# Performance work log

Hardware: AMD Instinct MI355X
Metric: run time of the kernel (lower is better)

Reference implementation:

```python
import jax, jax.numpy as jnp
import numpy as np

DEPTH, DIM, HEADS, MLP_HID, POS_DIM, PROJ_DIM, NCLS, INP = 5, 128, 8, 256, 128, 128, 1000, 35
EPS = 1e-5

def _ln(x, g, b):
    m = x.mean(-1, keepdims=True)
    v = ((x - m) ** 2).mean(-1, keepdims=True)
    return (x - m) / jnp.sqrt(v + EPS) * g + b

def _gelu(x):
    return jax.nn.gelu(x, approximate=False)  # torch nn.GELU default (erf)

def setup_inputs() -> dict:
    key = jax.random.key(0)
    ks = iter(jax.random.split(key, 80))
    nxt = lambda: next(ks)
    B, N = 8, 1024
    w = lambda *s: (jax.random.normal(nxt(), s, jnp.float32) / np.sqrt(s[-2]).astype(np.float32))
    z = lambda *s: jnp.zeros(s, jnp.float32)
    o = lambda *s: jnp.ones(s, jnp.float32)
    node_feat = jax.random.normal(nxt(), (B, N, 3), jnp.float32)
    a = (jax.random.uniform(nxt(), (B, N, N)) < 0.01).astype(jnp.float32)
    adj = jnp.maximum(a, a.transpose(0, 2, 1))  # symmetric 0/1 adjacency
    lapl = jax.random.normal(nxt(), (B, N, 32), jnp.float32) * 0.1
    d = dict(
        node_feat=node_feat, adj=adj, lapl=lapl,
        cls_token=jax.random.normal(nxt(), (1, 1, DIM), jnp.float32),
        pe_w1=w(INP, 2 * INP), pe_b1=z(2 * INP),
        pe_w2=w(2 * INP, 2 * INP), pe_b2=z(2 * INP),
        pe_w3=w(2 * INP, 2 * INP), pe_b3=z(2 * INP),
        pe_lng=o(2 * INP), pe_lnb=z(2 * INP),
        pe_w4=w(2 * INP, POS_DIM), pe_b4=z(POS_DIM),
        blk_ln1_g=o(DEPTH, DIM), blk_ln1_b=z(DEPTH, DIM),
        blk_qkv_w=w(DEPTH, DIM, 3 * HEADS * DIM),
        blk_proj_w=w(DEPTH, HEADS * DIM, DIM), blk_proj_b=z(DEPTH, DIM),
        blk_gamma_w=jax.random.uniform(nxt(), (DEPTH, DIM, 2), jnp.float32) * 0.01,
        blk_gamma_b=z(DEPTH, 2),
        blk_ln2_g=o(DEPTH, DIM), blk_ln2_b=z(DEPTH, DIM),
        blk_mlp_w1=w(DEPTH, DIM, MLP_HID), blk_mlp_b1=z(DEPTH, MLP_HID),
        blk_mlp_w2=w(DEPTH, MLP_HID, DIM), blk_mlp_b2=z(DEPTH, DIM),
        head_lng=o(DIM), head_lnb=z(DIM), head_w=w(DIM, DIM), head_b=z(DIM),
        proj_w1=w(DIM, PROJ_DIM), proj_b1=z(PROJ_DIM),
        proj_w2=w(PROJ_DIM, PROJ_DIM), proj_b2=z(PROJ_DIM),
        proj_w3=w(PROJ_DIM, PROJ_DIM), proj_b3=z(PROJ_DIM),
        proj_lng=o(PROJ_DIM), proj_lnb=z(PROJ_DIM),
        proj_w4=w(PROJ_DIM, NCLS), proj_b4=z(NCLS),
    )
    return d

def reference(node_feat, adj, lapl, cls_token, pe_w1, pe_b1, pe_w2, pe_b2, pe_w3, pe_b3,
              pe_lng, pe_lnb, pe_w4, pe_b4, blk_ln1_g, blk_ln1_b, blk_qkv_w, blk_proj_w,
              blk_proj_b, blk_gamma_w, blk_gamma_b, blk_ln2_g, blk_ln2_b, blk_mlp_w1,
              blk_mlp_b1, blk_mlp_w2, blk_mlp_b2, head_lng, head_lnb, head_w, head_b,
              proj_w1, proj_b1, proj_w2, proj_b2, proj_w3, proj_b3, proj_lng, proj_lnb,
              proj_w4, proj_b4):
    B, N, _ = node_feat.shape
    M = N + 1
    # positional-encoding MLP on concatenated [node_feat | lapl] (inp_dim = 35)
    x = jnp.concatenate([node_feat, lapl], axis=2)
    x = _gelu(x @ pe_w1 + pe_b1)
    x = _gelu(x @ pe_w2 + pe_b2)
    x = _gelu(x @ pe_w3 + pe_b3)
    x = _ln(x, pe_lng, pe_lnb) @ pe_w4 + pe_b4  # [B,N,DIM]
    x = jnp.concatenate([jnp.broadcast_to(cls_token, (B, 1, DIM)), x], axis=1)  # [B,M,DIM]
    # adjacency with cls row/col, adj_cls[:,0,0] = 1
    adj_cls = jnp.zeros((B, M, M), x.dtype).at[:, 0, 0].set(1.0).at[:, 1:, 1:].set(adj)
    scale = DIM ** (-0.5)
    for i in range(DEPTH):
        h = _ln(x, blk_ln1_g[i], blk_ln1_b[i])
        qkv = (h @ blk_qkv_w[i]).reshape(B, M, 3, HEADS, DIM).transpose(2, 0, 3, 1, 4)
        q, k, v = qkv[0], qkv[1], qkv[2]  # each [B,H,M,D]
        attn = jnp.einsum('bhnd,bhmd->bhnm', q, k) * scale
        gamma = jnp.exp(h @ blk_gamma_w[i] + blk_gamma_b[i])  # [B,M,2], use_exp=True
        attn = gamma[:, None, :, 0:1] * attn + gamma[:, None, :, 1:2] * adj_cls[:, None]
        attn = jax.nn.softmax(attn, axis=-1)
        o = jnp.einsum('bhnm,bhmd->bhnd', attn, v).transpose(0, 2, 1, 3).reshape(B, M, HEADS * DIM)
        x = o @ blk_proj_w[i] + blk_proj_b[i] + h  # residual from normed input (as in source)
        h2 = _ln(x, blk_ln2_g[i], blk_ln2_b[i])
        x = _gelu(h2 @ blk_mlp_w1[i] + blk_mlp_b1[i]) @ blk_mlp_w2[i] + blk_mlp_b2[i] + h2
    c = x[:, 0]
    c = _ln(c, head_lng, head_lnb) @ head_w + head_b  # mlp_head
    p = _gelu(c @ proj_w1 + proj_b1)
    p = _gelu(p @ proj_w2 + proj_b2)
    p = _gelu(p @ proj_w3 + proj_b3)
    p = _ln(p, proj_lng, proj_lnb) @ proj_w4 + proj_b4
    return (c, p)
```

## Files before the change

### kernel.cpp

```cpp
#include <hip/hip_runtime.h>
#include <hip/hip_bf16.h>
#include <math.h>

#define NB 8
#define NSEQ 1024
#define M_ 1025
#define ROWS (NB * M_)
#define DIMC 128
#define NHEADS 8
#define QKV3 3072
#define PEROWS (NB * NSEQ)
#define ACS 1088

typedef __attribute__((ext_vector_type(8))) short bf16x8;
typedef __attribute__((ext_vector_type(4))) float f32x4;

__device__ __forceinline__ float gelu_f(float x) {
  return 0.5f * x * (1.f + erff(x * 0.70710678118654752440f));
}

__device__ __forceinline__ unsigned short f2bf(float f) {
  __hip_bfloat16 h = __float2bfloat16(f);
  return *reinterpret_cast<unsigned short*>(&h);
}

__device__ __forceinline__ float bf2f(unsigned short u) {
  union { unsigned int i; float f; } c;
  c.i = ((unsigned int)u) << 16;
  return c.f;
}

__device__ __forceinline__ void g2lds16(const void* g, void* l) {
  __builtin_amdgcn_global_load_lds(
      (__attribute__((address_space(1))) void*)(g),
      (__attribute__((address_space(3))) void*)(l), 16, 0, 0);
}

template<int K, int KP, int C, int SS, int DOGELU>
__device__ __forceinline__ void pe_stage(
    int tid, const float* __restrict__ W, const float* __restrict__ B,
    const float* src, float* dst, float (*wb)[128])
{
  for (int i = tid; i < K * C; i += 128) wb[i / C][i % C] = W[i];
  if (tid < C) {
#pragma unroll
    for (int k = K; k < KP; ++k) wb[k][tid] = 0.f;
  }
  __syncthreads();
  if (tid < C) {
    float acc[16];
#pragma unroll
    for (int r = 0; r < 16; ++r) acc[r] = B[tid];
#pragma unroll 1
    for (int k4 = 0; k4 < KP; k4 += 4) {
      const float w0 = wb[k4 + 0][tid];
      const float w1 = wb[k4 + 1][tid];
      const float w2 = wb[k4 + 2][tid];
      const float w3 = wb[k4 + 3][tid];
#pragma unroll
      for (int r = 0; r < 16; ++r) {
        const float4 av = *(const float4*)&src[r * SS + k4];
        acc[r] = fmaf(av.x, w0, acc[r]);
        acc[r] = fmaf(av.y, w1, acc[r]);
        acc[r] = fmaf(av.z, w2, acc[r]);
        acc[r] = fmaf(av.w, w3, acc[r]);
      }
    }
#pragma unroll
    for (int r = 0; r < 16; ++r) dst[r * 72 + tid] = DOGELU ? gelu_f(acc[r]) : acc[r];
  }
  __syncthreads();
}

__global__ __launch_bounds__(128) void pe_fused_k(
    const float* __restrict__ nf, const float* __restrict__ lp,
    const float* __restrict__ w1, const float* __restrict__ b1,
    const float* __restrict__ w2, const float* __restrict__ b2,
    const float* __restrict__ w3, const float* __restrict__ b3,
    const float* __restrict__ lng, const float* __restrict__ lnb,
    const float* __restrict__ w4, const float* __restrict__ b4,
    float* __restrict__ x)
{
  __shared__ float sIn[16][36];
  __shared__ float sX[16][72];
  __shared__ float sY[16][72];
  __shared__ float wb[72][128];
  const int tid = threadIdx.x;
  const int r0 = blockIdx.x * 16;

  for (int i = tid; i < 16 * 35; i += 128) {
    const int r = i / 35, c = i - r * 35;
    const int gr = r0 + r;
    sIn[r][c] = (c < 3) ? nf[(size_t)gr * 3 + c] : lp[(size_t)gr * 32 + (c - 3)];
  }
  if (tid < 16) {
    sIn[tid][35] = 0.f;
    sX[tid][70] = 0.f; sX[tid][71] = 0.f;
    sY[tid][70] = 0.f; sY[tid][71] = 0.f;
  }
  __syncthreads();

  pe_stage<35, 36, 70, 36, 1>(tid, w1, b1, &sIn[0][0], &sX[0][0], wb);
  pe_stage<70, 72, 70, 72, 1>(tid, w2, b2, &sX[0][0], &sY[0][0], wb);
  pe_stage<70, 72, 70, 72, 1>(tid, w3, b3, &sY[0][0], &sX[0][0], wb);

  if (tid < 16) {
    float m = 0.f;
    for (int d = 0; d < 70; ++d) m += sX[tid][d];
    m *= (1.f / 70.f);
    float v = 0.f;
    for (int d = 0; d < 70; ++d) { const float t = sX[tid][d] - m; v += t * t; }
    const float inv = rsqrtf(v * (1.f / 70.f) + 1e-5f);
    for (int d = 0; d < 70; ++d) sX[tid][d] = (sX[tid][d] - m) * inv * lng[d] + lnb[d];
  }
  __syncthreads();

  {
    for (int i = tid; i < 70 * 128; i += 128) wb[i >> 7][i & 127] = w4[i];
#pragma unroll
    for (int k = 70; k < 72; ++k) wb[k][tid] = 0.f;
    __syncthreads();
    float acc[16];
#pragma unroll
    for (int r = 0; r < 16; ++r) acc[r] = b4[tid];
#pragma unroll 1
    for (int k4 = 0; k4 < 72; k4 += 4) {
      const float w0 = wb[k4 + 0][tid];
      const float w1v = wb[k4 + 1][tid];
      const float w2v = wb[k4 + 2][tid];
      const float w3v = wb[k4 + 3][tid];
#pragma unroll
      for (int r = 0; r < 16; ++r) {
        const float4 av = *(const float4*)&sX[r][k4];
        acc[r] = fmaf(av.x, w0, acc[r]);
        acc[r] = fmaf(av.y, w1v, acc[r]);
        acc[r] = fmaf(av.z, w2v, acc[r]);
        acc[r] = fmaf(av.w, w3v, acc[r]);
      }
    }
#pragma unroll
    for (int r = 0; r < 16; ++r) {
      const int gr = r0 + r;
      x[(size_t)(gr + gr / 1024 + 1) * DIMC + tid] = acc[r];
    }
  }
}

template<int ACT, int OBF, int RES>
__global__ __launch_bounds__(256) void mgemm_k(
    const unsigned short* __restrict__ Xb, const unsigned short* __restrict__ Wt,
    const float* __restrict__ bias, const float* __restrict__ res,
    void* __restrict__ outp, int rows, int K, int N)
{
  __shared__ unsigned short sX[64][72];
  __shared__ unsigned short sW[64][72];
  const int tid = threadIdx.x;
  const int w = tid >> 6, lane = tid & 63;
  const int col = lane & 15, quad = lane >> 4;
  const int r0 = blockIdx.x * 64, n0 = blockIdx.y * 64;
  const int lr = tid >> 2, lc = tid & 3;
  const int xrow = min(r0 + lr, rows - 1);
  const unsigned short* xsrc = Xb + (size_t)xrow * K + lc * 8;
  const unsigned short* wsrc = Wt + (size_t)(n0 + lr) * K + lc * 8;

  f32x4 acc[4];
#pragma unroll
  for (int t = 0; t < 4; ++t) acc[t] = (f32x4){0.f, 0.f, 0.f, 0.f};

  for (int k0 = 0; k0 < K; k0 += 64) {
    __syncthreads();
    *(uint4*)&sX[lr][lc * 8]      = *(const uint4*)(xsrc + k0);
    *(uint4*)&sX[lr][lc * 8 + 32] = *(const uint4*)(xsrc + k0 + 32);
    *(uint4*)&sW[lr][lc * 8]      = *(const uint4*)(wsrc + k0);
    *(uint4*)&sW[lr][lc * 8 + 32] = *(const uint4*)(wsrc + k0 + 32);
    __syncthreads();
    const bf16x8 aX0 = *(const bf16x8*)&sX[w * 16 + col][quad * 8];
    const bf16x8 aX1 = *(const bf16x8*)&sX[w * 16 + col][32 + quad * 8];
#pragma unroll
    for (int t = 0; t < 4; ++t) {
      const bf16x8 bW0 = *(const bf16x8*)&sW[t * 16 + col][quad * 8];
      const bf16x8 bW1 = *(const bf16x8*)&sW[t * 16 + col][32 + quad * 8];
      acc[t] = __builtin_amdgcn_mfma_f32_16x16x32_bf16(aX0, bW0, acc[t], 0, 0, 0);
      acc[t] = __builtin_amdgcn_mfma_f32_16x16x32_bf16(aX1, bW1, acc[t], 0, 0, 0);
    }
  }
  const int gr_base = r0 + w * 16 + quad * 4;
#pragma unroll
  for (int t = 0; t < 4; ++t) {
    const int n = n0 + t * 16 + col;
    const float bv = bias ? bias[n] : 0.f;
#pragma unroll
    for (int r = 0; r < 4; ++r) {
      const int gr = gr_base + r;
      if (gr < rows) {
        float v = acc[t][r] + bv;
        if (ACT) v = gelu_f(v);
        if (RES) v += res[(size_t)gr * N + n];
        if (OBF) ((unsigned short*)outp)[(size_t)gr * N + n] = f2bf(v);
        else     ((float*)outp)[(size_t)gr * N + n] = v;
      }
    }
  }
}

template<int OBF, int VT>
__global__ __launch_bounds__(256) void mgemm128_k(
    const unsigned short* __restrict__ Xb, const unsigned short* __restrict__ Wt,
    const float* __restrict__ bias, void* __restrict__ outp,
    unsigned short* __restrict__ vtp, int rows, int K, int N)
{
  __shared__ unsigned short sX[128][72];
  __shared__ unsigned short sW[128][72];
  const int tid = threadIdx.x;
  const int w = tid >> 6, lane = tid & 63;
  const int col = lane & 15, quad = lane >> 4;
  const int wr = w >> 1, wc = w & 1;
  const int r0 = blockIdx.x * 128, n0 = blockIdx.y * 128;

  f32x4 acc[4][4];
#pragma unroll
  for (int i = 0; i < 4; ++i)
#pragma unroll
    for (int j = 0; j < 4; ++j) acc[i][j] = (f32x4){0.f, 0.f, 0.f, 0.f};

  for (int k0 = 0; k0 < K; k0 += 64) {
    __syncthreads();
#pragma unroll
    for (int l = 0; l < 4; ++l) {
      const int idx = l * 256 + tid;
      const int row = idx >> 3, c = idx & 7;
      const int xrow = min(r0 + row, rows - 1);
      *(uint4*)&sX[row][c * 8] = *(const uint4*)(Xb + (size_t)xrow * K + k0 + c * 8);
      *(uint4*)&sW[row][c * 8] = *(const uint4*)(Wt + (size_t)(n0 + row) * K + k0 + c * 8);
    }
    __syncthreads();
    bf16x8 aX[4][2];
#pragma unroll
    for (int i = 0; i < 4; ++i) {
      aX[i][0] = *(const bf16x8*)&sX[wr * 64 + i * 16 + col][quad * 8];
      aX[i][1] = *(const bf16x8*)&sX[wr * 64 + i * 16 + col][32 + quad * 8];
    }
#pragma unroll
    for (int j = 0; j < 4; ++j) {
      const bf16x8 b0 = *(const bf16x8*)&sW[wc * 64 + j * 16 + col][quad * 8];
      const bf16x8 b1 = *(const bf16x8*)&sW[wc * 64 + j * 16 + col][32 + quad * 8];
#pragma unroll
      for (int i = 0; i < 4; ++i) {
        acc[i][j] = __builtin_amdgcn_mfma_f32_16x16x32_bf16(aX[i][0], b0, acc[i][j], 0, 0, 0);
        acc[i][j] = __builtin_amdgcn_mfma_f32_16x16x32_bf16(aX[i][1], b1, acc[i][j], 0, 0, 0);
      }
    }
  }
  const bool dovt = VT && (n0 >= 2048);
#pragma unroll
  for (int i = 0; i < 4; ++i) {
    const int gr_base = r0 + wr * 64 + i * 16 + quad * 4;
    int bb[4], mm[4];
    if (dovt) {
#pragma unroll
      for (int r = 0; r < 4; ++r) {
        const int gr = gr_base + r;
        bb[r] = gr / 1025;
        mm[r] = gr - bb[r] * 1025;
      }
    }
#pragma unroll
    for (int j = 0; j < 4; ++j) {
      const int n = n0 + wc * 64 + j * 16 + col;
      const float bv = bias ? bias[n] : 0.f;
      const int hh = (n - 2048) >> 7;
      const int d  = (n - 2048) & 127;
#pragma unroll
      for (int r = 0; r < 4; ++r) {
        const int gr = gr_base + r;
        if (gr < rows) {
          const float v = acc[i][j][r] + bv;
          const unsigned short bf = f2bf(v);
          if (OBF) ((unsigned short*)outp)[(size_t)gr * N + n] = bf;
          else     ((float*)outp)[(size_t)gr * N + n] = v;
          if (dovt) vtp[(((size_t)(bb[r] * NHEADS + hh) * DIMC + d) * ACS) + mm[r]] = bf;
        }
      }
    }
  }
}

__global__ __launch_bounds__(256) void ln_rows_k(
    const float* __restrict__ in, float* __restrict__ out,
    unsigned short* __restrict__ outb,
    const float* __restrict__ g, const float* __restrict__ b,
    const float* __restrict__ gw, const float* __restrict__ gb,
    float* __restrict__ gamout, int rows, int D)
{
  const int wv = (blockIdx.x * blockDim.x + threadIdx.x) >> 6;
  const int lane = threadIdx.x & 63;
  if (wv >= rows) return;
  const float* r = in + (size_t)wv * D;
  float s = 0.f;
  for (int d = lane; d < D; d += 64) s += r[d];
  for (int off = 32; off; off >>= 1) s += __shfl_down(s, off);
  const float mean = __shfl(s, 0) / (float)D;
  float v = 0.f;
  for (int d = lane; d < D; d += 64) { float t = r[d] - mean; v += t * t; }
  for (int off = 32; off; off >>= 1) v += __shfl_down(v, off);
  const float inv = rsqrtf(__shfl(v, 0) / (float)D + 1e-5f);
  float* orow = out + (size_t)wv * D;
  float a0 = 0.f, a1 = 0.f;
  for (int d = lane; d < D; d += 64) {
    const float o = (r[d] - mean) * inv * g[d] + b[d];
    orow[d] = o;
    if (outb) outb[(size_t)wv * D + d] = f2bf(o);
    if (gw) { a0 = fmaf(o, gw[2 * d], a0); a1 = fmaf(o, gw[2 * d + 1], a1); }
  }
  if (gw) {
    for (int off = 32; off; off >>= 1) { a0 += __shfl_down(a0, off); a1 += __shfl_down(a1, off); }
    if (lane == 0) {
      gamout[(size_t)wv * 2 + 0] = expf(a0 + gb[0]);
      gamout[(size_t)wv * 2 + 1] = expf(a1 + gb[1]);
    }
  }
}

__global__ __launch_bounds__(256) void adjp_k(const float* __restrict__ adj,
                                              unsigned long long* __restrict__ adjp)
{
  const int n = blockIdx.x;
  const int b = blockIdx.y;
  const int wv = threadIdx.x >> 6, lane = threadIdx.x & 63;
  for (int w = wv; w < 17; w += 4) {
    const int m = w * 64 + lane;
    float av = 0.f;
    if (n == 0) av = (m == 0) ? 1.f : 0.f;
    else if (m >= 1 && m <= NSEQ) av = adj[((size_t)b * NSEQ + (n - 1)) * NSEQ + (m - 1)];
    const unsigned long long mask = __ballot(av != 0.f);
    if (lane == 0) adjp[((size_t)b * M_ + n) * 17 + w] = mask;
  }
}

__global__ void wtrans_k(const float* __restrict__ W, unsigned short* __restrict__ Wt,
                         int K, int N)
{
  __shared__ float t[32][33];
  const int k0 = blockIdx.x * 32, n0 = blockIdx.y * 32;
  const float* Wd = W + (size_t)blockIdx.z * K * N;
  unsigned short* Wtd = Wt + (size_t)blockIdx.z * K * N;
  for (int i = threadIdx.y; i < 32; i += 8)
    t[i][threadIdx.x] = Wd[(size_t)(k0 + i) * N + n0 + threadIdx.x];
  __syncthreads();
  for (int i = threadIdx.y; i < 32; i += 8)
    Wtd[(size_t)(n0 + i) * K + k0 + threadIdx.x] = f2bf(t[threadIdx.x][i]);
}

__global__ __launch_bounds__(512) void attn_mfma_k(
    const unsigned short* __restrict__ qkv, const float* __restrict__ gamma,
    const unsigned long long* __restrict__ adjp, const unsigned short* __restrict__ vt,
    unsigned short* __restrict__ o)
{
  __shared__ unsigned short sK[2][64][128];
  __shared__ unsigned short sVt[2][128][64];
  __shared__ unsigned short sP[256][64];

  const int hh = blockIdx.x, qt = blockIdx.y, b = blockIdx.z;
  const int tid = threadIdx.x;
  const int w = tid >> 6;
  const int lane = tid & 63;
  const int col = lane & 15;
  const int quad = lane >> 4;
  const int qbase = qt * 256 + w * 32;
  const float scale = 0.088388347648318447f;

  bf16x8 aQ[2][4];
#pragma unroll
  for (int rg = 0; rg < 2; ++rg) {
    const int qrow = qbase + rg * 16 + col;
    const unsigned short* qp = qkv + ((size_t)(b * M_ + qrow)) * QKV3 + hh * DIMC + quad * 8;
#pragma unroll
    for (int c = 0; c < 4; ++c) aQ[rg][c] = *(const bf16x8*)(qp + c * 32);
  }
  float g0[2][4], g1[2][4];
  int adjo[2][4];
#pragma unroll
  for (int rg = 0; rg < 2; ++rg)
#pragma unroll
    for (int r = 0; r < 4; ++r) {
      const int nc = qbase + rg * 16 + quad * 4 + r;
      g0[rg][r] = gamma[(size_t)(b * M_ + nc) * 2 + 0] * scale;
      g1[rg][r] = gamma[(size_t)(b * M_ + nc) * 2 + 1];
      adjo[rg][r] = (b * M_ + nc) * 17;
    }

  float l_i[2][4] = {{0.f, 0.f, 0.f, 0.f}, {0.f, 0.f, 0.f, 0.f}};
  f32x4 Oacc[2][8];
#pragma unroll
  for (int rg = 0; rg < 2; ++rg)
#pragma unroll
    for (int t = 0; t < 8; ++t) Oacc[rg][t] = (f32x4){0.f, 0.f, 0.f, 0.f};

  const size_t vtbase = ((size_t)(b * NHEADS + hh)) * DIMC * ACS;

  auto stageK = [&](int buf, int kt_) {
#pragma unroll
    for (int l = 0; l < 2; ++l) {
      const int m = l * 32 + w * 4 + (lane >> 4);
      const int gm = min(kt_ * 64 + m, 1024);
      const unsigned short* src = qkv + ((size_t)(b * M_ + gm)) * QKV3 + 1024
                                  + hh * DIMC + (((lane & 15) ^ (m & 7)) * 8);
      g2lds16(src, &sK[buf][l * 32 + w * 4][0]);
    }
  };
  auto stageV = [&](int buf, int kt_) {
#pragma unroll
    for (int l = 0; l < 2; ++l) {
      const int d = l * 64 + w * 8 + (lane >> 3);
      const unsigned short* src = vt + vtbase + (size_t)d * ACS + kt_ * 64
                                  + (((lane & 7) ^ (d & 7)) * 8);
      g2lds16(src, &sVt[buf][l * 64 + w * 8][0]);
    }
  };

  stageK(0, 0);
  stageV(0, 0);

  int cur = 0;
  for (int kt = 0; kt < 17; ++kt) {
    const int m0 = kt * 64;
    asm volatile("s_waitcnt vmcnt(0)" ::: "memory");
    __builtin_amdgcn_s_barrier();
    __builtin_amdgcn_sched_barrier(0);

    const bool more = (kt < 16);
    if (more) {
      stageK(cur ^ 1, kt + 1);
      stageV(cur ^ 1, kt + 1);
    }

    unsigned long long mk[2][4];
#pragma unroll
    for (int rg = 0; rg < 2; ++rg)
#pragma unroll
      for (int r = 0; r < 4; ++r) mk[rg][r] = adjp[adjo[rg][r] + kt];

    f32x4 Sacc[2][4];
#pragma unroll
    for (int rg = 0; rg < 2; ++rg)
#pragma unroll
      for (int t = 0; t < 4; ++t) Sacc[rg][t] = (f32x4){0.f, 0.f, 0.f, 0.f};
    __builtin_amdgcn_s_setprio(1);
#pragma unroll
    for (int t = 0; t < 4; ++t) {
#pragma unroll
      for (int c = 0; c < 4; ++c) {
        const bf16x8 bK = *(const bf16x8*)&sK[cur][t * 16 + col][((c * 4 + quad) ^ (col & 7)) * 8];
        Sacc[0][t] = __builtin_amdgcn_mfma_f32_16x16x32_bf16(aQ[0][c], bK, Sacc[0][t], 0, 0, 0);
        Sacc[1][t] = __builtin_amdgcn_mfma_f32_16x16x32_bf16(aQ[1][c], bK, Sacc[1][t], 0, 0, 0);
      }
    }
    __builtin_amdgcn_s_setprio(0);

#pragma unroll
    for (int t = 0; t < 4; ++t) {
      const int m = m0 + t * 16 + col;
      const bool mv = (m < M_);
      const int chb = t * 2 + (col >> 3);
      const int sh = t * 16 + col;
#pragma unroll
      for (int rg = 0; rg < 2; ++rg)
#pragma unroll
        for (int r = 0; r < 4; ++r) {
          const float bias = ((mk[rg][r] >> sh) & 1ull) ? g1[rg][r] : 0.f;
          const float s = fmaf(g0[rg][r], Sacc[rg][t][r], bias);
          const float pv = mv ? __expf(s) : 0.f;
          l_i[rg][r] += pv;
          const int ql = w * 32 + rg * 16 + quad * 4 + r;
          sP[ql][((chb ^ (ql & 7)) * 8) + (col & 7)] = f2bf(pv);
        }
    }

    __builtin_amdgcn_s_setprio(1);
#pragma unroll
    for (int ch = 0; ch < 2; ++ch) {
      const int pr = w * 32 + col;
      const bf16x8 aP0 = *(const bf16x8*)&sP[pr][((ch * 4 + quad) ^ (col & 7)) * 8];
      const bf16x8 aP1 = *(const bf16x8*)&sP[pr + 16][((ch * 4 + quad) ^ (col & 7)) * 8];
#pragma unroll
      for (int t = 0; t < 8; ++t) {
        const bf16x8 bV = *(const bf16x8*)&sVt[cur][t * 16 + col][((ch * 4 + quad) ^ (col & 7)) * 8];
        Oacc[0][t] = __builtin_amdgcn_mfma_f32_16x16x32_bf16(aP0, bV, Oacc[0][t], 0, 0, 0);
        Oacc[1][t] = __builtin_amdgcn_mfma_f32_16x16x32_bf16(aP1, bV, Oacc[1][t], 0, 0, 0);
      }
    }
    __builtin_amdgcn_s_setprio(0);
    cur ^= 1;
  }

#pragma unroll
  for (int rg = 0; rg < 2; ++rg)
#pragma unroll
    for (int r = 0; r < 4; ++r) {
      float s = l_i[rg][r];
      s += __shfl_xor(s, 1);
      s += __shfl_xor(s, 2);
      s += __shfl_xor(s, 4);
      s += __shfl_xor(s, 8);
      const int n = qbase + rg * 16 + quad * 4 + r;
      const float invl = 1.f / s;
      unsigned short* orow = o + ((size_t)(b * M_ + n)) * (NHEADS * DIMC) + hh * DIMC + col;
#pragma unroll
      for (int t = 0; t < 8; ++t) orow[t * 16] = f2bf(Oacc[rg][t][r] * invl);
    }
}

__global__ __launch_bounds__(256) void cls_attn_k(
    const unsigned short* __restrict__ qkv, const float* __restrict__ gamma,
    const unsigned long long* __restrict__ adjp, const unsigned short* __restrict__ vt,
    unsigned short* __restrict__ o)
{
  __shared__ float qf[DIMC];
  __shared__ float pbuf[1056];
  __shared__ float lred[4];
  __shared__ float oshare[DIMC];
  const int hh = blockIdx.x & 7, b = blockIdx.x >> 3;
  const int tid = threadIdx.x;
  const size_t rowbase = (size_t)b * M_ + 1024;

  if (tid < DIMC) qf[tid] = bf2f(qkv[rowbase * QKV3 + hh * DIMC + tid]);
  __syncthreads();
  const float g0 = gamma[rowbase * 2 + 0] * 0.088388347648318447f;
  const float g1 = gamma[rowbase * 2 + 1];

  float lpart = 0.f;
  for (int m = tid; m < M_; m += 256) {
    const unsigned short* kp = qkv + ((size_t)(b * M_ + m)) * QKV3 + 1024 + hh * DIMC;
    float s = 0.f;
#pragma unroll
    for (int d0 = 0; d0 < DIMC; d0 += 8) {
      const bf16x8 kv = *(const bf16x8*)(kp + d0);
#pragma unroll
      for (int j = 0; j < 8; ++j)
        s = fmaf(bf2f((unsigned short)kv[j]), qf[d0 + j], s);
    }
    const unsigned long long mkv = adjp[rowbase * 17 + (m >> 6)];
    const float bias = ((mkv >> (m & 63)) & 1ull) ? g1 : 0.f;
    const float p = __expf(fmaf(g0, s, bias));
    pbuf[m] = p;
    lpart += p;
  }
  for (int off = 32; off; off >>= 1) lpart += __shfl_down(lpart, off);
  if ((tid & 63) == 0) lred[tid >> 6] = lpart;
  __syncthreads();
  const float linv = 1.f / (lred[0] + lred[1] + lred[2] + lred[3]);

  const int d = tid & 127, half = tid >> 7;
  const unsigned short* vrow = vt + ((size_t)(b * NHEADS + hh)) * DIMC * ACS + (size_t)d * ACS;
  float acc = 0.f;
  const int mstart = half * 512;
  const int mend = half ? 1024 : 512;
  for (int m0 = mstart; m0 < mend; m0 += 8) {
    const bf16x8 vv = *(const bf16x8*)(vrow + m0);
#pragma unroll
    for (int j = 0; j < 8; ++j)
      acc = fmaf(bf2f((unsigned short)vv[j]), pbuf[m0 + j], acc);
  }
  if (half) acc = fmaf(bf2f(vrow[1024]), pbuf[1024], acc);
  if (half == 0) oshare[d] = acc;
  __syncthreads();
  if (half == 1) {
    const float val = (oshare[d] + acc) * linv;
    o[rowbase * (NHEADS * DIMC) + hh * DIMC + d] = f2bf(val);
  }
}

template<int DOLN, int ACT>
__global__ __launch_bounds__(256) void hstage_k(
    const float* __restrict__ in, int in_stride,
    const float* __restrict__ lng, const float* __restrict__ lnb,
    const float* __restrict__ W, const float* __restrict__ bias,
    float* __restrict__ out)
{
  __shared__ float xn[8][128];
  __shared__ float red[128];
  const int tid = threadIdx.x;
  for (int i = tid; i < 1024; i += 256) {
    const int r = i >> 7, d = i & 127;
    xn[r][d] = in[(size_t)r * in_stride + d];
  }
  __syncthreads();
  if (DOLN) {
    const int wv = tid >> 6, lane = tid & 63;
    const int row = wv * 2 + (lane >> 5);
    const int l32 = lane & 31;
    float s = 0.f;
    for (int d = l32; d < 128; d += 32) s += xn[row][d];
    for (int off = 16; off; off >>= 1) s += __shfl_xor(s, off);
    const float mean = s * (1.f / 128.f);
    float v = 0.f;
    for (int d = l32; d < 128; d += 32) { const float t = xn[row][d] - mean; v += t * t; }
    for (int off = 16; off; off >>= 1) v += __shfl_xor(v, off);
    const float inv = rsqrtf(v * (1.f / 128.f) + 1e-5f);
    for (int d = l32; d < 128; d += 32)
      xn[row][d] = (xn[row][d] - mean) * inv * lng[d] + lnb[d];
    __syncthreads();
  }
  const int col = blockIdx.x * 16 + (tid & 15);
  const int row = (tid >> 4) & 7;
  const int ks = tid >> 7;
  float acc = 0.f;
  const int kb = ks * 64;
  for (int k = kb; k < kb + 64; ++k)
    acc = fmaf(xn[row][k], W[k * 128 + col], acc);
  if (ks) red[tid - 128] = acc;
  __syncthreads();
  if (!ks) {
    float v = acc + red[tid] + bias[col];
    if (ACT) v = gelu_f(v);
    out[row * 128 + col] = v;
  }
}

__global__ __launch_bounds__(256) void hfinal_k(
    const float* __restrict__ in,
    const float* __restrict__ plg, const float* __restrict__ plb,
    const float* __restrict__ W, const float* __restrict__ bias,
    float* __restrict__ out_p)
{
  __shared__ float xn[128];
  const int r = blockIdx.x & 7, cc = blockIdx.x >> 3;
  const int tid = threadIdx.x;
  const int lane = tid & 63;
  const float a = in[r * 128 + lane];
  const float b = in[r * 128 + 64 + lane];
  float s = a + b;
  for (int off = 32; off; off >>= 1) s += __shfl_xor(s, off);
  const float mean = s * (1.f / 128.f);
  const float t0 = a - mean, t1 = b - mean;
  float v = t0 * t0 + t1 * t1;
  for (int off = 32; off; off >>= 1) v += __shfl_xor(v, off);
  const float inv = rsqrtf(v * (1.f / 128.f) + 1e-5f);
  if (tid < 128) xn[tid] = (in[r * 128 + tid] - mean) * inv * plg[tid] + plb[tid];
  __syncthreads();
  const int col = cc * 250 + tid;
  if (tid < 250) {
    float acc = bias[col];
    for (int k = 0; k < 128; ++k)
      acc = fmaf(xn[k], W[(size_t)k * 1000 + col], acc);
    out_p[r * 1000 + col] = acc;
  }
}

__global__ void fill_cls_k(const float* __restrict__ cls, float* __restrict__ x)
{
  x[(size_t)blockIdx.x * M_ * DIMC + threadIdx.x] = cls[threadIdx.x];
}

extern "C" void kernel_launch(void* const* d_in, const int* in_sizes, int n_in,
                              void* d_out, int out_size, void* d_ws, size_t ws_size,
                              hipStream_t stream)
{
  (void)in_sizes; (void)n_in; (void)out_size; (void)ws_size;
  const float* node_feat = (const float*)d_in[0];
  const float* adj       = (const float*)d_in[1];
  const float* lapl      = (const float*)d_in[2];
  const float* cls_token = (const float*)d_in[3];
  const float* pe_w1 = (const float*)d_in[4];
  const float* pe_b1 = (const float*)d_in[5];
  const float* pe_w2 = (const float*)d_in[6];
  const float* pe_b2 = (const float*)d_in[7];
  const float* pe_w3 = (const float*)d_in[8];
  const float* pe_b3 = (const float*)d_in[9];
  const float* pe_lng = (const float*)d_in[10];
  const float* pe_lnb = (const float*)d_in[11];
  const float* pe_w4 = (const float*)d_in[12];
  const float* pe_b4 = (const float*)d_in[13];
  const float* blk_ln1_g = (const float*)d_in[14];
  const float* blk_ln1_b = (const float*)d_in[15];
  const float* blk_qkv_w = (const float*)d_in[16];
  const float* blk_proj_w = (const float*)d_in[17];
  const float* blk_proj_b = (const float*)d_in[18];
  const float* blk_gamma_w = (const float*)d_in[19];
  const float* blk_gamma_b = (const float*)d_in[20];
  const float* blk_ln2_g = (const float*)d_in[21];
  const float* blk_ln2_b = (const float*)d_in[22];
  const float* blk_mlp_w1 = (const float*)d_in[23];
  const float* blk_mlp_b1 = (const float*)d_in[24];
  const float* blk_mlp_w2 = (const float*)d_in[25];
  const float* blk_mlp_b2 = (const float*)d_in[26];
  const float* head_lng = (const float*)d_in[27];
  const float* head_lnb = (const float*)d_in[28];
  const float* head_w = (const float*)d_in[29];
  const float* head_b = (const float*)d_in[30];
  const float* proj_w1 = (const float*)d_in[31];
  const float* proj_b1 = (const float*)d_in[32];
  const float* proj_w2 = (const float*)d_in[33];
  const float* proj_b2 = (const float*)d_in[34];
  const float* proj_w3 = (const float*)d_in[35];
  const float* proj_b3 = (const float*)d_in[36];
  const float* proj_lng = (const float*)d_in[37];
  const float* proj_lnb = (const float*)d_in[38];
  const float* proj_w4 = (const float*)d_in[39];
  const float* proj_b4 = (const float*)d_in[40];

  float* ws   = (float*)d_ws;
  float* x    = ws;
  float* h    = x + 1049600;
  float* gam  = h + 1049600;
  float* obuf = gam + 16400;
  unsigned short* obufb = (unsigned short*)obuf;
  unsigned short* hidb  = (unsigned short*)(obuf + 4198400);
  float* sm  = obuf + 5248000;
  unsigned short* hb   = (unsigned short*)(sm + 8192);
  unsigned short* qkv  = hb + 1049600;
  unsigned long long* adjp = (unsigned long long*)(qkv + 25190400);
  unsigned short* vt   = (unsigned short*)(adjp + 139400 + 88);
  unsigned short* qkvWt = vt + 8912896;
  unsigned short* projWt = qkvWt + 5 * 393216;
  unsigned short* mlp1Wt = projWt + 5 * 131072;
  unsigned short* mlp2Wt = mlp1Wt + 5 * 32768;

  float* out_c = (float*)d_out;
  float* out_p = out_c + NB * DIMC;
  float* p1 = sm;
  float* p2 = sm + 1024;

  adjp_k<<<dim3(M_, NB), 256, 0, stream>>>(adj, adjp);
  wtrans_k<<<dim3(4, 96, 5), dim3(32, 8), 0, stream>>>(blk_qkv_w, qkvWt, 128, 3072);
  wtrans_k<<<dim3(32, 4, 5), dim3(32, 8), 0, stream>>>(blk_proj_w, projWt, 1024, 128);
  wtrans_k<<<dim3(4, 8, 5), dim3(32, 8), 0, stream>>>(blk_mlp_w1, mlp1Wt, 128, 256);
  wtrans_k<<<dim3(8, 4, 5), dim3(32, 8), 0, stream>>>(blk_mlp_w2, mlp2Wt, 256, 128);

  pe_fused_k<<<512, 128, 0, stream>>>(node_feat, lapl, pe_w1, pe_b1, pe_w2, pe_b2,
                                      pe_w3, pe_b3, pe_lng, pe_lnb, pe_w4, pe_b4, x);
  fill_cls_k<<<NB, DIMC, 0, stream>>>(cls_token, x);

  const int lnGrid = (ROWS * 64 + 255) / 256;
  for (int i = 0; i < 5; ++i) {
    const float* ln1g = blk_ln1_g + i * DIMC;
    const float* ln1b = blk_ln1_b + i * DIMC;
    const float* pb   = blk_proj_b + i * DIMC;
    const float* gw   = blk_gamma_w + (size_t)i * DIMC * 2;
    const float* gb   = blk_gamma_b + i * 2;
    const float* ln2g = blk_ln2_g + i * DIMC;
    const float* ln2b = blk_ln2_b + i * DIMC;
    const float* mb1  = blk_mlp_b1 + i * 256;
    const float* mb2  = blk_mlp_b2 + i * DIMC;
    const unsigned short* qw = qkvWt + (size_t)i * 393216;
    const unsigned short* pw = projWt + (size_t)i * 131072;
    const unsigned short* m1w = mlp1Wt + (size_t)i * 32768;
    const unsigned short* m2w = mlp2Wt + (size_t)i * 32768;

    ln_rows_k<<<lnGrid, 256, 0, stream>>>(x, h, hb, ln1g, ln1b, gw, gb, gam, ROWS, DIMC);
    mgemm128_k<1, 1><<<dim3(65, 24), 256, 0, stream>>>(hb, qw, nullptr, qkv, vt, ROWS, 128, 3072);
    attn_mfma_k<<<dim3(NHEADS, 4, NB), 512, 0, stream>>>(qkv, gam, adjp, vt, obufb);
    cls_attn_k<<<64, 256, 0, stream>>>(qkv, gam, adjp, vt, obufb);
    mgemm_k<0, 0, 1><<<dim3(129, 2), 256, 0, stream>>>(obufb, pw, pb, h, x, ROWS, 1024, 128);
    ln_rows_k<<<lnGrid, 256, 0, stream>>>(x, h, hb, ln2g, ln2b, nullptr, nullptr, nullptr, ROWS, DIMC);
    mgemm_k<1, 1, 0><<<dim3(129, 4), 256, 0, stream>>>(hb, m1w, mb1, nullptr, hidb, ROWS, 128, 256);
    mgemm_k<0, 0, 1><<<dim3(129, 2), 256, 0, stream>>>(hidb, m2w, mb2, h, x, ROWS, 256, 128);
  }

  hstage_k<1, 0><<<8, 256, 0, stream>>>(x, M_ * DIMC, head_lng, head_lnb,
                                        head_w, head_b, out_c);
  hstage_k<0, 1><<<8, 256, 0, stream>>>(out_c, 128, nullptr, nullptr,
                                        proj_w1, proj_b1, p1);
  hstage_k<0, 1><<<8, 256, 0, stream>>>(p1, 128, nullptr, nullptr,
                                        proj_w2, proj_b2, p2);
  hstage_k<0, 1><<<8, 256, 0, stream>>>(p2, 128, nullptr, nullptr,
                                        proj_w3, proj_b3, p1);
  hfinal_k<<<32, 256, 0, stream>>>(p1, proj_lng, proj_lnb, proj_w4, proj_b4, out_p);
}
```

Baseline: 1.350 ms.

## Fuse LayerNorm and gamma projection into proj and MLP2 GEMM epilogues

Adds a GEMM kernel that computes the full 128-wide output row per block, so it can apply bias and residual and then do the row LayerNorm with wave shuffles. For the next block it also computes the exp gamma projection in the same epilogue. This replaces the separate LayerNorm kernels and the fp32 round trip of x between stages, leaving one LN launch before the loop. In exchange, the proj and MLP2 GEMMs run on 129 blocks instead of 258, which lowers parallelism, notably for the K=1024 projection.

Result: no change. 1.374 ms (+1.7%).

```diff
diff --git a/kernel.cpp b/kernel.cpp
--- a/kernel.cpp
+++ b/kernel.cpp
@@ -198,6 +198,124 @@
         if (RES) v += res[(size_t)gr * N + n];
         if (OBF) ((unsigned short*)outp)[(size_t)gr * N + n] = f2bf(v);
         else     ((float*)outp)[(size_t)gr * N + n] = v;
+      }
+    }
+  }
+}
+
+template<int DOLN, int GAMMA, int WRITEX>
+__global__ __launch_bounds__(256) void mgemm_ln_k(
+    const unsigned short* __restrict__ Xb, const unsigned short* __restrict__ Wt,
+    const float* __restrict__ bias, const float* __restrict__ res,
+    const float* __restrict__ lng, const float* __restrict__ lnb,
+    const float* __restrict__ gw, const float* __restrict__ gb,
+    float* __restrict__ xout, float* __restrict__ h,
+    unsigned short* __restrict__ hb, float* __restrict__ gamout,
+    int rows, int K)
+{
+  __shared__ unsigned short sX[64][72];
+  __shared__ unsigned short sW[128][72];
+  const int tid = threadIdx.x;
+  const int w = tid >> 6, lane = tid & 63;
+  const int col = lane & 15, quad = lane >> 4;
+  const int r0 = blockIdx.x * 64;
+
+  f32x4 acc[8];
+#pragma unroll
+  for (int t = 0; t < 8; ++t) acc[t] = (f32x4){0.f, 0.f, 0.f, 0.f};
+
+  for (int k0 = 0; k0 < K; k0 += 64) {
+    __syncthreads();
+#pragma unroll
+    for (int l = 0; l < 2; ++l) {
+      const int idx = l * 256 + tid;
+      const int row = idx >> 3, c = idx & 7;
+      const int xrow = min(r0 + row, rows - 1);
+      *(uint4*)&sX[row][c * 8] = *(const uint4*)(Xb + (size_t)xrow * K + k0 + c * 8);
+    }
+#pragma unroll
+    for (int l = 0; l < 4; ++l) {
+      const int idx = l * 256 + tid;
+      const int row = idx >> 3, c = idx & 7;
+      *(uint4*)&sW[row][c * 8] = *(const uint4*)(Wt + (size_t)row * K + k0 + c * 8);
+    }
+    __syncthreads();
+    const bf16x8 aX0 = *(const bf16x8*)&sX[w * 16 + col][quad * 8];
+    const bf16x8 aX1 = *(const bf16x8*)&sX[w * 16 + col][32 + quad * 8];
+#pragma unroll
+    for (int t = 0; t < 8; ++t) {
+      const bf16x8 bW0 = *(const bf16x8*)&sW[t * 16 + col][quad * 8];
+      const bf16x8 bW1 = *(const bf16x8*)&sW[t * 16 + col][32 + quad * 8];
+      acc[t] = __builtin_amdgcn_mfma_f32_16x16x32_bf16(aX0, bW0, acc[t], 0, 0, 0);
+      acc[t] = __builtin_amdgcn_mfma_f32_16x16x32_bf16(aX1, bW1, acc[t], 0, 0, 0);
+    }
+  }
+
+  const int gr_base = r0 + w * 16 + quad * 4;
+  float bv[8];
+#pragma unroll
+  for (int t = 0; t < 8; ++t) bv[t] = bias[t * 16 + col];
+  float val[8][4];
+#pragma unroll
+  for (int r = 0; r < 4; ++r) {
+    const int grc = min(gr_base + r, rows - 1);
+#pragma unroll
+    for (int t = 0; t < 8; ++t)
+      val[t][r] = acc[t][r] + bv[t] + res[(size_t)grc * DIMC + t * 16 + col];
+  }
+  if (WRITEX) {
+#pragma unroll
+    for (int r = 0; r < 4; ++r) {
+      const int gr = gr_base + r;
+      if (gr < rows) {
+#pragma unroll
+        for (int t = 0; t < 8; ++t)
+          xout[(size_t)gr * DIMC + t * 16 + col] = val[t][r];
+      }
+    }
+  }
+  if (DOLN) {
+    float lg[8], lb[8], gwa[8], gwb[8];
+#pragma unroll
+    for (int t = 0; t < 8; ++t) {
+      lg[t] = lng[t * 16 + col];
+      lb[t] = lnb[t * 16 + col];
+      if (GAMMA) { gwa[t] = gw[2 * (t * 16 + col)]; gwb[t] = gw[2 * (t * 16 + col) + 1]; }
+    }
+#pragma unroll
+    for (int r = 0; r < 4; ++r) {
+      const int gr = gr_base + r;
+      float s = 0.f;
+#pragma unroll
+      for (int t = 0; t < 8; ++t) s += val[t][r];
+      s += __shfl_xor(s, 1); s += __shfl_xor(s, 2);
+      s += __shfl_xor(s, 4); s += __shfl_xor(s, 8);
+      const float mean = s * (1.f / 128.f);
+      float vv = 0.f;
+#pragma unroll
+      for (int t = 0; t < 8; ++t) { const float d = val[t][r] - mean; vv += d * d; }
+      vv += __shfl_xor(vv, 1); vv += __shfl_xor(vv, 2);
+      vv += __shfl_xor(vv, 4); vv += __shfl_xor(vv, 8);
+      const float inv = rsqrtf(vv * (1.f / 128.f) + 1e-5f);
+      float a0 = 0.f, a1 = 0.f;
+#pragma unroll
+      for (int t = 0; t < 8; ++t) {
+        const float o = (val[t][r] - mean) * inv * lg[t] + lb[t];
+        if (gr < rows) {
+          h[(size_t)gr * DIMC + t * 16 + col] = o;
+          hb[(size_t)gr * DIMC + t * 16 + col] = f2bf(o);
+        }
+        if (GAMMA) { a0 = fmaf(o, gwa[t], a0); a1 = fmaf(o, gwb[t], a1); }
+      }
+      if (GAMMA) {
+        a0 += __shfl_xor(a0, 1); a0 += __shfl_xor(a0, 2);
+        a0 += __shfl_xor(a0, 4); a0 += __shfl_xor(a0, 8);
+        a1 += __shfl_xor(a1, 1); a1 += __shfl_xor(a1, 2);
+        a1 += __shfl_xor(a1, 4); a1 += __shfl_xor(a1, 8);
+        if (col == 0 && gr < rows) {
+          gamout[(size_t)gr * 2 + 0] = expf(a0 + gb[0]);
+          gamout[(size_t)gr * 2 + 1] = expf(a1 + gb[1]);
+        }
       }
     }
   }
@@ -732,12 +850,11 @@
   fill_cls_k<<<NB, DIMC, 0, stream>>>(cls_token, x);
 
   const int lnGrid = (ROWS * 64 + 255) / 256;
+  ln_rows_k<<<lnGrid, 256, 0, stream>>>(x, h, hb, blk_ln1_g, blk_ln1_b,
+                                        blk_gamma_w, blk_gamma_b, gam, ROWS, DIMC);
+
   for (int i = 0; i < 5; ++i) {
-    const float* ln1g = blk_ln1_g + i * DIMC;
-    const float* ln1b = blk_ln1_b + i * DIMC;
     const float* pb   = blk_proj_b + i * DIMC;
-    const float* gw   = blk_gamma_w + (size_t)i * DIMC * 2;
-    const float* gb   = blk_gamma_b + i * 2;
     const float* ln2g = blk_ln2_g + i * DIMC;
     const float* ln2b = blk_ln2_b + i * DIMC;
     const float* mb1  = blk_mlp_b1 + i * 256;
@@ -747,14 +864,29 @@
     const unsigned short* m1w = mlp1Wt + (size_t)i * 32768;
     const unsigned short* m2w = mlp2Wt + (size_t)i * 32768;
 
-    ln_rows_k<<<lnGrid, 256, 0, stream>>>(x, h, hb, ln1g, ln1b, gw, gb, gam, ROWS, DIMC);
     mgemm128_k<1, 1><<<dim3(65, 24), 256, 0, stream>>>(hb, qw, nullptr, qkv, vt, ROWS, 128, 3072);
     attn_mfma_k<<<dim3(NHEADS, 4, NB), 512, 0, stream>>>(qkv, gam, adjp, vt, obufb);
     cls_attn_k<<<64, 256, 0, stream>>>(qkv, gam, adjp, vt, obufb);
-    mgemm_k<0, 0, 1><<<dim3(129, 2), 256, 0, stream>>>(obufb, pw, pb, h, x, ROWS, 1024, 128);
-    ln_rows_k<<<lnGrid, 256, 0, stream>>>(x, h, hb, ln2g, ln2b, nullptr, nullptr, nullptr, ROWS, DIMC);
+
+    mgemm_ln_k<1, 0, 0><<<129, 256, 0, stream>>>(
+        obufb, pw, pb, h, ln2g, ln2b, nullptr, nullptr,
+        nullptr, h, hb, nullptr, ROWS, 1024);
+
     mgemm_k<1, 1, 0><<<dim3(129, 4), 256, 0, stream>>>(hb, m1w, mb1, nullptr, hidb, ROWS, 128, 256);
-    mgemm_k<0, 0, 1><<<dim3(129, 2), 256, 0, stream>>>(hidb, m2w, mb2, h, x, ROWS, 256, 128);
+
+    if (i < 4) {
+      const float* nln1g = blk_ln1_g + (i + 1) * DIMC;
+      const float* nln1b = blk_ln1_b + (i + 1) * DIMC;
+      const float* ngw   = blk_gamma_w + (size_t)(i + 1) * DIMC * 2;
+      const float* ngb   = blk_gamma_b + (i + 1) * 2;
+      mgemm_ln_k<1, 1, 0><<<129, 256, 0, stream>>>(
+          hidb, m2w, mb2, h, nln1g, nln1b, ngw, ngb,
+          nullptr, h, hb, gam, ROWS, 256);
+    } else {
+      mgemm_ln_k<0, 0, 1><<<129, 256, 0, stream>>>(
+          hidb, m2w, mb2, h, nullptr, nullptr, nullptr, nullptr,
+          x, nullptr, nullptr, nullptr, ROWS, 256);
+    }
   }
 
   hstage_k<1, 0><<<8, 256, 0, stream>>>(x, M_ * DIMC, head_lng, head_lnb,
```
